# Kernel optimization log

Measured on AMD Instinct MI355X. Metric: run time of the kernel, lower is better.

Reference implementation:

```python
import jax, jax.numpy as jnp
import numpy as np

VOCAB = 32000
EMB = 512
HID = 1024
B = 64
LPRE = 256
MAXL = 16


def _gru(x, Wih, Whh, bih, bhh):
    # x: (B, T, E); torch GRU gate order r, z, n
    Bb, T, E = x.shape
    H = Whh.shape[1]
    xW = jnp.einsum('bte,ge->btg', x, Wih) + bih  # (B, T, 3H)
    def step(h, xt):
        gh = h @ Whh.T + bhh
        r = jax.nn.sigmoid(xt[:, :H] + gh[:, :H])
        z = jax.nn.sigmoid(xt[:, H:2 * H] + gh[:, H:2 * H])
        n = jnp.tanh(xt[:, 2 * H:] + r * gh[:, 2 * H:])
        h = (1.0 - z) * n + z * h
        return h, h
    h0 = jnp.zeros((Bb, H), x.dtype)
    hT, ys = jax.lax.scan(step, h0, jnp.swapaxes(xW, 0, 1))
    return jnp.swapaxes(ys, 0, 1), hT


def setup_inputs() -> dict:
    key = jax.random.key(0)
    ks = jax.random.split(key, 24)
    s = 0.02
    inp = {
        'pre_seq': jax.random.randint(ks[0], (B, LPRE), 0, VOCAB),
        'post_seq': jax.random.randint(ks[1], (B, LPRE), 0, VOCAB),
        'trg': jax.random.randint(ks[2], (B, MAXL), 0, 2),
        'emb': jax.random.normal(ks[3], (VOCAB, EMB), jnp.float32) * s,
        'Wih_pre': jax.random.normal(ks[4], (3 * HID, EMB), jnp.float32) * s,
        'Whh_pre': jax.random.normal(ks[5], (3 * HID, HID), jnp.float32) * s,
        'bih_pre': jnp.zeros((3 * HID,), jnp.float32),
        'bhh_pre': jnp.zeros((3 * HID,), jnp.float32),
        'Wih_post': jax.random.normal(ks[6], (3 * HID, EMB), jnp.float32) * s,
        'Whh_post': jax.random.normal(ks[7], (3 * HID, HID), jnp.float32) * s,
        'bih_post': jnp.zeros((3 * HID,), jnp.float32),
        'bhh_post': jnp.zeros((3 * HID,), jnp.float32),
        'fc_W': jax.random.normal(ks[8], (HID, 2 * HID), jnp.float32) * s,
        'fc_b': jnp.zeros((HID,), jnp.float32),
        'attn_W': jax.random.normal(ks[9], (HID, 2 * HID), jnp.float32) * s,
        'attn_b': jnp.zeros((HID,), jnp.float32),
        'v_W': jax.random.normal(ks[10], (1, HID), jnp.float32) * s,
        'fc1_W': jax.random.normal(ks[11], (HID, HID), jnp.float32) * s,
        'fc1_b': jnp.zeros((HID,), jnp.float32),
        'fc2_W': jax.random.normal(ks[12], (HID, 2 * HID), jnp.float32) * s,
        'fc2_b': jnp.zeros((HID,), jnp.float32),
        'fco_W': jax.random.normal(ks[13], (1, 2 * HID), jnp.float32) * s,
        'fco_b': jnp.zeros((1,), jnp.float32),
    }
    return inp


def reference(pre_seq, post_seq, trg, emb,
              Wih_pre, Whh_pre, bih_pre, bhh_pre,
              Wih_post, Whh_post, bih_post, bhh_post,
              fc_W, fc_b, attn_W, attn_b, v_W,
              fc1_W, fc1_b, fc2_W, fc2_b, fco_W, fco_b):
    bsz, len_pre = pre_seq.shape
    max_len = trg.shape[1]
    # Encoder (dropout = identity, eval mode)
    pre_e = emb[pre_seq]
    post_e = emb[post_seq]
    pre_out, pre_h = _gru(pre_e, Wih_pre, Whh_pre, bih_pre, bhh_pre)
    post_out, post_h = _gru(post_e, Wih_post, Whh_post, bih_post, bhh_post)
    enc_out = jnp.concatenate([pre_out, post_out], axis=1)  # (B, 2*Lp, H)
    hidden = jnp.tanh(jnp.concatenate([pre_h, post_h], axis=-1) @ fc_W.T + fc_b)  # (B, H)
    # Decoder: hidden is never updated in the original loop, so one step suffices;
    # the per-t result is identical and is broadcast over max_len.
    src_len = enc_out.shape[1]
    hid_rep = jnp.broadcast_to(hidden[:, None, :], (bsz, src_len, hidden.shape[-1]))
    energy = jnp.tanh(jnp.concatenate([hid_rep, enc_out], axis=-1) @ attn_W.T + attn_b)
    a = jax.nn.softmax(jnp.einsum('bsh,h->bs', energy, v_W[0]), axis=1)  # (B, S)
    weighted = jnp.einsum('bs,bsh->bh', a, enc_out)  # (B, H)
    o = jnp.tanh(hidden @ fc1_W.T + fc1_b)
    o = jnp.tanh(jnp.concatenate([o, weighted], axis=1) @ fc2_W.T + fc2_b)  # (B, H)
    o_rep = jnp.broadcast_to(o[:, None, :], (bsz, src_len, o.shape[-1]))
    feat = jax.nn.relu(jnp.concatenate([enc_out, o_rep], axis=-1))  # (B, S, 2H)
    logits = jnp.einsum('bsf,of->bso', feat, fco_W) + fco_b  # (B, S, 1)
    sig = jax.nn.sigmoid(logits)
    outputs_pre = jnp.broadcast_to(sig[:, None, :len_pre, :], (bsz, max_len, len_pre, 1))
    outputs_post = jnp.broadcast_to(sig[:, None, len_pre:, :], (bsz, max_len, len_pre, 1))
    return outputs_pre, outputs_post
```

## Files before the change

### kernel.cpp

```cpp
#include <hip/hip_runtime.h>
#include <math.h>

#define BATCH 64
#define LPRE 256
#define EMBD 512
#define HID 1024
#define G3 3072
#define SRC 512

typedef unsigned int uint32;
typedef unsigned long long u64;
typedef short bf16x8 __attribute__((ext_vector_type(8)));
typedef float f32x4 __attribute__((ext_vector_type(4)));
typedef uint32 u32x4 __attribute__((ext_vector_type(4)));

__device__ __forceinline__ float frcp_(float x) { return __builtin_amdgcn_rcpf(x); }
__device__ __forceinline__ float sigmoidf_(float x) {
    x = fminf(fmaxf(x, -30.f), 30.f);
    return frcp_(1.0f + __expf(-x));
}
__device__ __forceinline__ float tanhf_(float x) {
    x = fminf(fmaxf(x, -15.f), 15.f);
    float e = __expf(2.f * x);
    return (e - 1.f) * frcp_(e + 1.f);
}

__device__ __forceinline__ unsigned short f2bf(float f) {
    uint32 u = __float_as_uint(f);
    return (unsigned short)((u + 0x7fffu + ((u >> 16) & 1u)) >> 16);
}
__device__ __forceinline__ float bf2f(unsigned short s) { return __uint_as_float(((uint32)s) << 16); }
__device__ __forceinline__ void up2(uint32 u, float& f0, float& f1) {
    f0 = __uint_as_float(u << 16);
    f1 = __uint_as_float(u & 0xffff0000u);
}
__device__ __forceinline__ uint4 pack8(float4 a, float4 b) {
    uint4 w;
    w.x = (uint32)f2bf(a.x) | ((uint32)f2bf(a.y) << 16);
    w.y = (uint32)f2bf(a.z) | ((uint32)f2bf(a.w) << 16);
    w.z = (uint32)f2bf(b.x) | ((uint32)f2bf(b.y) << 16);
    w.w = (uint32)f2bf(b.z) | ((uint32)f2bf(b.w) << 16);
    return w;
}

__global__ __launch_bounds__(256) void kcvt(const float* __restrict__ src, int ld, int off,
                                            unsigned short* __restrict__ dst, int cols, int n) {
    int i = blockIdx.x * 256 + threadIdx.x;
    if (i >= n) return;
    int r = i / cols, c = i - r * cols;
    dst[i] = f2bf(src[(size_t)r * ld + off + c]);
}

__global__ __launch_bounds__(256) void kproj(const int* __restrict__ pre_seq,
                                             const int* __restrict__ post_seq, int t0,
                                             const float* __restrict__ emb,
                                             const unsigned short* __restrict__ Wihb,
                                             const float* __restrict__ bih_pre,
                                             const float* __restrict__ bih_post,
                                             unsigned short* __restrict__ xw, int chunk) {
    __shared__ uint4 Asl[4][128];
    __shared__ uint4 Bsl[4][128];
    __shared__ int tok[128];
    int gru = blockIdx.z;
    const int* seq = gru ? post_seq : pre_seq;
    const unsigned short* Wb = Wihb + (size_t)gru * G3 * EMBD;
    const float* bih = gru ? bih_post : bih_pre;
    unsigned short* xwout = xw + (size_t)gru * BATCH * chunk * G3;
    int tid = threadIdx.x;
    int row0 = blockIdx.x * 128, col0 = blockIdx.y * 128;
    if (tid < 128) {
        int rr = row0 + tid;
        tok[tid] = seq[(rr / chunk) * LPRE + t0 + (rr % chunk)];
    }
    __syncthreads();
    int lane = tid & 63, w = tid >> 6;
    int wm = w >> 1, wn = w & 1;
    int q = lane >> 4, m = lane & 15;
    int r0s = tid & 127, g0s = tid >> 7;
    int g1s = g0s + 2;
    f32x4 acc[4][4] = {};
    for (int kk = 0; kk < EMBD; kk += 32) {
        const float* a0p = emb + (size_t)tok[r0s] * EMBD + kk + g0s * 8;
        const float* a1p = emb + (size_t)tok[r0s] * EMBD + kk + g1s * 8;
        float4 av00 = *(const float4*)a0p, av01 = *(const float4*)(a0p + 4);
        float4 av10 = *(const float4*)a1p, av11 = *(const float4*)(a1p + 4);
        uint4 bv0 = *(const uint4*)(Wb + (size_t)(col0 + r0s) * EMBD + kk + g0s * 8);
        uint4 bv1 = *(const uint4*)(Wb + (size_t)(col0 + r0s) * EMBD + kk + g1s * 8);
        __syncthreads();
        Asl[g0s][r0s ^ (g0s << 2)] = pack8(av00, av01);
        Asl[g1s][r0s ^ (g1s << 2)] = pack8(av10, av11);
        Bsl[g0s][r0s ^ (g0s << 2)] = bv0;
        Bsl[g1s][r0s ^ (g1s << 2)] = bv1;
        __syncthreads();
        bf16x8 af[4], bfv[4];
#pragma unroll
        for (int i = 0; i < 4; i++) af[i] = *(bf16x8*)&Asl[q][(wm * 64 + i * 16 + m) ^ (q << 2)];
#pragma unroll
        for (int j = 0; j < 4; j++) bfv[j] = *(bf16x8*)&Bsl[q][(wn * 64 + j * 16 + m) ^ (q << 2)];
#pragma unroll
        for (int i = 0; i < 4; i++)
#pragma unroll
            for (int j = 0; j < 4; j++)
                acc[i][j] = __builtin_amdgcn_mfma_f32_16x16x32_bf16(af[i], bfv[j], acc[i][j], 0, 0, 0);
    }
#pragma unroll
    for (int i = 0; i < 4; i++)
#pragma unroll
        for (int j = 0; j < 4; j++)
#pragma unroll
            for (int reg = 0; reg < 4; reg++) {
                int row = row0 + wm * 64 + i * 16 + q * 4 + reg;
                int col = col0 + wn * 64 + j * 16 + m;
                xwout[(size_t)row * G3 + col] = f2bf(acc[i][j][reg] + bih[col]);
            }
}

__global__ __launch_bounds__(512, 2) void kstepP(unsigned short* __restrict__ hbp,
                                                 float* __restrict__ hf,
                                                 const unsigned short* __restrict__ Whhb,
                                                 const float* __restrict__ bhh0,
                                                 const float* __restrict__ bhh1,
                                                 const unsigned short* __restrict__ xw,
                                                 unsigned short* __restrict__ enc,
                                                 uint32* __restrict__ bar,
                                                 int t0, int chunk) {
    __shared__ float gl[8][32][3][17];
    __shared__ unsigned short hsh[32][16];
    int gru = blockIdx.z;
    int mh = blockIdx.y;
    int u0 = blockIdx.x * 16;
    int tid = threadIdx.x;
    int ks = tid >> 6;
    int lane = tid & 63;
    int q = lane >> 4, m = lane & 15;
    int bbase = mh * 32;
    const unsigned short* Wg = Whhb + (size_t)gru * G3 * HID;
    const float* bhh = gru ? bhh1 : bhh0;

    int dom = gru * 2 + mh;
    uint32* slots = bar + (size_t)dom * 128;
    uint32* gen = bar + 512 + (size_t)dom * 32;
    int sid = blockIdx.x;
    bool leader = (blockIdx.x == 0);

    bf16x8 bfrag[3][4];
#pragma unroll
    for (int g = 0; g < 3; ++g) {
        const unsigned short* pb = Wg + (size_t)(g * HID + u0 + m) * HID + ks * 128 + q * 8;
#pragma unroll
        for (int it = 0; it < 4; ++it) bfrag[g][it] = *(const bf16x8*)(pb + it * 32);
    }
#pragma unroll
    for (int g = 0; g < 3; ++g)
#pragma unroll
        for (int it = 0; it < 4; ++it) asm volatile("" : "+v"(bfrag[g][it]));

    int bl = tid >> 4, ul = tid & 15;
    int be = bbase + bl, ue = u0 + ul;
    float brr = bhh[ue], bzz = bhh[HID + ue], bnn = bhh[2 * HID + ue];
    unsigned short h16r = __hip_atomic_load(
        &hbp[(size_t)(((t0 & 1) * 2 + gru) * BATCH + be) * HID + ue],
        __ATOMIC_RELAXED, __HIP_MEMORY_SCOPE_AGENT);

    const unsigned short* xwb = xw + ((size_t)(gru * BATCH + be) * chunk) * G3;
    float xr = bf2f(xwb[ue]);
    float xz = bf2f(xwb[HID + ue]);
    float xn = bf2f(xwb[2 * HID + ue]);

    for (int tl = 0; tl < chunk; ++tl) {
        int t = t0 + tl;
        int p = t & 1;
        const unsigned short* hb = hbp + ((size_t)p * 2 + gru) * BATCH * HID;
        unsigned short* hob = hbp + ((size_t)(p ^ 1) * 2 + gru) * BATCH * HID;

        const unsigned short* pa0 = hb + (size_t)(bbase + m) * HID + ks * 128 + q * 8;
        const unsigned short* pa1 = pa0 + (size_t)16 * HID;
        u32x4 av0[4], av1[4];
#pragma unroll
        for (int it = 0; it < 4; ++it) {
            asm volatile("global_load_dwordx4 %0, %1, off sc0 sc1"
                         : "=v"(av0[it]) : "v"(pa0 + it * 32));
            asm volatile("global_load_dwordx4 %0, %1, off sc0 sc1"
                         : "=v"(av1[it]) : "v"(pa1 + it * 32));
        }
        asm volatile("s_waitcnt vmcnt(0)" ::: "memory");
        __builtin_amdgcn_sched_barrier(0);

        f32x4 acc[3][2] = {};
#pragma unroll
        for (int it = 0; it < 4; ++it)
#pragma unroll
            for (int g = 0; g < 3; ++g) {
                acc[g][0] = __builtin_amdgcn_mfma_f32_16x16x32_bf16(*(bf16x8*)&av0[it], bfrag[g][it], acc[g][0], 0, 0, 0);
                acc[g][1] = __builtin_amdgcn_mfma_f32_16x16x32_bf16(*(bf16x8*)&av1[it], bfrag[g][it], acc[g][1], 0, 0, 0);
            }
#pragma unroll
        for (int g = 0; g < 3; ++g)
#pragma unroll
            for (int reg = 0; reg < 4; ++reg) {
                gl[ks][q * 4 + reg][g][m] = acc[g][0][reg];
                gl[ks][16 + q * 4 + reg][g][m] = acc[g][1][reg];
            }
        __syncthreads();
        float ar = 0.f, az = 0.f, an = 0.f;
#pragma unroll
        for (int k2 = 0; k2 < 8; ++k2) {
            ar += gl[k2][bl][0][ul];
            az += gl[k2][bl][1][ul];
            an += gl[k2][bl][2][ul];
        }
        float r = sigmoidf_(xr + ar + brr);
        float z = sigmoidf_(xz + az + bzz);
        float n = tanhf_(xn + r * (an + bnn));
        float hnew = (1.f - z) * n + z * bf2f(h16r);
        unsigned short h16 = f2bf(hnew);
        h16r = h16;
        hsh[bl][ul] = h16;
        enc[((size_t)be * SRC + gru * LPRE + t) * HID + ue] = h16;
        if (t == LPRE - 1) hf[((size_t)gru * BATCH + be) * HID + ue] = hnew;
        __syncthreads();
        if (tid < 64) {
            int row = tid >> 1, half = tid & 1;
            u32x4 hv = *(const u32x4*)&hsh[row][half * 8];
            unsigned short* dst = hob + (size_t)(bbase + row) * HID + u0 + half * 8;
            asm volatile("global_store_dwordx4 %0, %1, off sc0 sc1"
                         :: "v"(dst), "v"(hv) : "memory");
        }
        if (tl < chunk - 1) {
            uint32 t1 = (uint32)(t + 1);
            if (tid < 64)
                asm volatile("s_waitcnt vmcnt(0)" ::: "memory");
            if (tid == 0)
                __hip_atomic_store(&slots[sid], t1, __ATOMIC_RELAXED, __HIP_MEMORY_SCOPE_AGENT);
            const unsigned short* xwn = xwb + (size_t)(tl + 1) * G3;
            xr = bf2f(xwn[ue]);
            xz = bf2f(xwn[HID + ue]);
            xn = bf2f(xwn[2 * HID + ue]);
            if (leader && tid < 64) {
                for (;;) {
                    uint32 s0 = __hip_atomic_load(&slots[tid], __ATOMIC_RELAXED, __HIP_MEMORY_SCOPE_AGENT);
                    if (__all(s0 >= t1)) break;
                    __builtin_amdgcn_s_sleep(1);
                }
                if (tid == 0)
                    __hip_atomic_store(gen, t1, __ATOMIC_RELAXED, __HIP_MEMORY_SCOPE_AGENT);
            }
            if (tid == 0) {
                while (__hip_atomic_load(gen, __ATOMIC_RELAXED, __HIP_MEMORY_SCOPE_AGENT) < t1)
                    __builtin_amdgcn_s_sleep(1);
            }
            __syncthreads();
        }
    }
}

__global__ __launch_bounds__(256) void kg64(const float* __restrict__ A1, int K1,
                                            const float* __restrict__ A2, int K2,
                                            const unsigned short* __restrict__ Wb,
                                            const float* __restrict__ bias,
                                            float* __restrict__ out, int N, int act) {
    __shared__ uint4 Asl[4][64];
    int tid = threadIdx.x;
    int col0 = blockIdx.x * 64;
    int lane = tid & 63, w = tid >> 6;
    int q = lane >> 4, m = lane & 15;
    int K = K1 + K2;
    int arow = tid >> 2, akg = tid & 3;
    const unsigned short* wp = Wb + (size_t)(col0 + w * 16 + m) * K + q * 8;
    f32x4 acc[4] = {};
    for (int kk = 0; kk < K; kk += 32) {
        int k0 = kk + akg * 8;
        const float* ap = (k0 < K1) ? (A1 + (size_t)arow * K1 + k0)
                                    : (A2 + (size_t)arow * K2 + (k0 - K1));
        float4 v0 = *(const float4*)ap;
        float4 v1 = *(const float4*)(ap + 4);
        __syncthreads();
        Asl[akg][arow ^ (akg << 2)] = pack8(v0, v1);
        __syncthreads();
        bf16x8 bfv = *(const bf16x8*)(wp + kk);
        bf16x8 af[4];
#pragma unroll
        for (int i = 0; i < 4; i++) af[i] = *(bf16x8*)&Asl[q][(i * 16 + m) ^ (q << 2)];
#pragma unroll
        for (int i = 0; i < 4; i++)
            acc[i] = __builtin_amdgcn_mfma_f32_16x16x32_bf16(af[i], bfv, acc[i], 0, 0, 0);
    }
    int j = col0 + w * 16 + m;
    float bv = bias ? bias[j] : 0.f;
#pragma unroll
    for (int i = 0; i < 4; i++)
#pragma unroll
        for (int reg = 0; reg < 4; reg++) {
            int b = i * 16 + q * 4 + reg;
            float v = acc[i][reg] + bv;
            if (act == 1) v = tanhf_(v);
            out[(size_t)b * N + j] = v;
        }
}

__global__ __launch_bounds__(256) void kattn(const unsigned short* __restrict__ enc,
                                             const unsigned short* __restrict__ Wb,
                                             const float* __restrict__ attn_b,
                                             const float* __restrict__ hidA,
                                             const float* __restrict__ vW,
                                             const float* __restrict__ fcoW,
                                             float* __restrict__ e,
                                             float* __restrict__ dvec) {
    __shared__ uint4 Asl[4][128];
    __shared__ uint4 Bsl[4][128];
    __shared__ float red[2][128][17];
    __shared__ float dred[128][2];
    __shared__ float fsh[HID];
    int tid = threadIdx.x;
    int row0 = blockIdx.x * 128, col0 = blockIdx.y * 128;
    bool dwork = (blockIdx.y == 0);
    if (dwork)
        for (int l = tid; l < HID; l += 256) fsh[l] = fcoW[l];
    int lane = tid & 63, w = tid >> 6;
    int wm = w >> 1, wn = w & 1;
    int q = lane >> 4, m = lane & 15;
    int r0s = tid & 127, g0s = tid >> 7;
    int g1s = g0s + 2;
    f32x4 acc[4][4] = {};
    float dacc = 0.f;
    for (int kk = 0; kk < HID; kk += 32) {
        uint4 av0 = *(const uint4*)(enc + (size_t)(row0 + r0s) * HID + kk + g0s * 8);
        uint4 av1 = *(const uint4*)(enc + (size_t)(row0 + r0s) * HID + kk + g1s * 8);
        uint4 bv0 = *(const uint4*)(Wb + (size_t)(col0 + r0s) * HID + kk + g0s * 8);
        uint4 bv1 = *(const uint4*)(Wb + (size_t)(col0 + r0s) * HID + kk + g1s * 8);
        __syncthreads();
        Asl[g0s][r0s ^ (g0s << 2)] = av0;
        Asl[g1s][r0s ^ (g1s << 2)] = av1;
        Bsl[g0s][r0s ^ (g0s << 2)] = bv0;
        Bsl[g1s][r0s ^ (g1s << 2)] = bv1;
        __syncthreads();
        bf16x8 af[4], bfv[4];
#pragma unroll
        for (int i = 0; i < 4; i++) af[i] = *(bf16x8*)&Asl[q][(wm * 64 + i * 16 + m) ^ (q << 2)];
#pragma unroll
        for (int j = 0; j < 4; j++) bfv[j] = *(bf16x8*)&Bsl[q][(wn * 64 + j * 16 + m) ^ (q << 2)];
        if (dwork) {
            int r2 = tid >> 1, sp = tid & 1;
#pragma unroll
            for (int sg = 0; sg < 2; sg++) {
                int seg = sp * 2 + sg;
                uint4 v = Asl[seg][r2 ^ (seg << 2)];
                const uint32* vw = (const uint32*)&v;
#pragma unroll
                for (int wd = 0; wd < 4; wd++) {
                    float e0, e1;
                    up2(vw[wd], e0, e1);
                    int kb = kk + seg * 8 + wd * 2;
                    dacc += fmaxf(e0, 0.f) * fsh[kb] + fmaxf(e1, 0.f) * fsh[kb + 1];
                }
            }
        }
#pragma unroll
        for (int i = 0; i < 4; i++)
#pragma unroll
            for (int j = 0; j < 4; j++)
                acc[i][j] = __builtin_amdgcn_mfma_f32_16x16x32_bf16(af[i], bfv[j], acc[i][j], 0, 0, 0);
    }
    int b = row0 / SRC;
#pragma unroll
    for (int i = 0; i < 4; i++)
#pragma unroll
        for (int reg = 0; reg < 4; reg++) {
            int row_local = wm * 64 + i * 16 + q * 4 + reg;
            float s = 0.f;
#pragma unroll
            for (int j = 0; j < 4; j++) {
                int col = col0 + wn * 64 + j * 16 + m;
                float v = acc[i][j][reg] + hidA[(size_t)b * HID + col] + attn_b[col];
                s += vW[col] * tanhf(v);
            }
            red[wn][row_local][m] = s;
        }
    if (dwork) dred[tid >> 1][tid & 1] = dacc;
    __syncthreads();
    if (tid < 128) {
        float s = 0.f;
        for (int c = 0; c < 16; c++) s += red[0][tid][c] + red[1][tid][c];
        atomicAdd(e + row0 + tid, s);
        if (dwork) dvec[row0 + tid] = dred[tid][0] + dred[tid][1];
    }
}

__global__ __launch_bounds__(256) void ksoftmax(const float* __restrict__ e, float* __restrict__ a) {
    int b = blockIdx.x;
    int tid = threadIdx.x;
    __shared__ float red[256];
    float v0 = e[(size_t)b * SRC + tid], v1 = e[(size_t)b * SRC + 256 + tid];
    red[tid] = fmaxf(v0, v1);
    __syncthreads();
    for (int st = 128; st > 0; st >>= 1) {
        if (tid < st) red[tid] = fmaxf(red[tid], red[tid + st]);
        __syncthreads();
    }
    float mx = red[0];
    __syncthreads();
    float e0 = __expf(v0 - mx), e1 = __expf(v1 - mx);
    red[tid] = e0 + e1;
    __syncthreads();
    for (int st = 128; st > 0; st >>= 1) {
        if (tid < st) red[tid] += red[tid + st];
        __syncthreads();
    }
    float inv = 1.0f / red[0];
    a[(size_t)b * SRC + tid] = e0 * inv;
    a[(size_t)b * SRC + 256 + tid] = e1 * inv;
}

__global__ __launch_bounds__(256) void kweighted(const float* __restrict__ a,
                                                 const unsigned short* __restrict__ enc,
                                                 float* __restrict__ wout) {
    int b = blockIdx.y;
    int h = blockIdx.x * 256 + threadIdx.x;
    __shared__ float as[512];
    for (int l = threadIdx.x; l < 512; l += 256) as[l] = a[(size_t)b * SRC + l];
    __syncthreads();
    float acc = 0.f;
    for (int s = 0; s < SRC; s++) acc += as[s] * bf2f(enc[((size_t)b * SRC + s) * HID + h]);
    wout[(size_t)b * HID + h] = acc;
}

__global__ __launch_bounds__(256) void koc(const float* __restrict__ o2,
                                           const float* __restrict__ fcoW,
                                           float* __restrict__ oc) {
    int b = blockIdx.x;
    int tid = threadIdx.x;
    __shared__ float red[256];
    float s = 0.f;
    for (int j = tid; j < HID; j += 256) s += fmaxf(o2[(size_t)b * HID + j], 0.f) * fcoW[HID + j];
    red[tid] = s;
    __syncthreads();
    for (int st = 128; st > 0; st >>= 1) {
        if (tid < st) red[tid] += red[tid + st];
        __syncthreads();
    }
    if (tid == 0) oc[b] = red[0];
}

__global__ __launch_bounds__(256) void kout(const float* __restrict__ dvec,
                                            const float* __restrict__ oc,
                                            const float* __restrict__ fcob,
                                            float* __restrict__ out) {
    int idx = blockIdx.x * 256 + threadIdx.x;
    int b = idx >> 9, s = idx & 511;
    float logit = dvec[idx] + oc[b] + fcob[0];
    float sig = frcp_(1.f + __expf(-fminf(fmaxf(logit, -30.f), 30.f)));
    size_t base = (s < LPRE) ? ((size_t)b * 4096 + s)
                             : (262144 + (size_t)b * 4096 + (s - 256));
    for (int l = 0; l < 16; l++) out[base + (size_t)l * 256] = sig;
}

extern "C" void kernel_launch(void* const* d_in, const int* in_sizes, int n_in,
                              void* d_out, int out_size, void* d_ws, size_t ws_size,
                              hipStream_t stream) {
    (void)in_sizes; (void)n_in; (void)out_size;
    const int* pre_seq = (const int*)d_in[0];
    const int* post_seq = (const int*)d_in[1];
    const float* emb = (const float*)d_in[3];
    const float* Wih_pre = (const float*)d_in[4];
    const float* Whh_pre = (const float*)d_in[5];
    const float* bih_pre = (const float*)d_in[6];
    const float* bhh_pre = (const float*)d_in[7];
    const float* Wih_post = (const float*)d_in[8];
    const float* Whh_post = (const float*)d_in[9];
    const float* bih_post = (const float*)d_in[10];
    const float* bhh_post = (const float*)d_in[11];
    const float* fc_W = (const float*)d_in[12];
    const float* fc_b = (const float*)d_in[13];
    const float* attn_W = (const float*)d_in[14];
    const float* attn_b = (const float*)d_in[15];
    const float* v_W = (const float*)d_in[16];
    const float* fc1_W = (const float*)d_in[17];
    const float* fc1_b = (const float*)d_in[18];
    const float* fc2_W = (const float*)d_in[19];
    const float* fc2_b = (const float*)d_in[20];
    const float* fco_W = (const float*)d_in[21];
    const float* fco_b = (const float*)d_in[22];
    float* out = (float*)d_out;

    const size_t fixed_bytes = 103420160ull + 65536;
    int CH = (ws_size >= fixed_bytes + (size_t)2 * BATCH * 64 * G3 * 2) ? 64 : 32;

    char* ws = (char*)d_ws;
    unsigned short* xw = (unsigned short*)ws;     ws += (size_t)2 * BATCH * CH * G3 * 2;
    unsigned short* enc = (unsigned short*)ws;    ws += (size_t)BATCH * SRC * HID * 2;
    unsigned short* hbp = (unsigned short*)ws;    ws += (size_t)2 * 2 * BATCH * HID * 2;
    float* hf = (float*)ws;                       ws += (size_t)2 * BATCH * HID * 4;
    unsigned short* Wihb = (unsigned short*)ws;   ws += (size_t)2 * G3 * EMBD * 2;
    unsigned short* Whhb = (unsigned short*)ws;   ws += (size_t)2 * G3 * HID * 2;
    unsigned short* attnWb = (unsigned short*)ws; ws += (size_t)HID * HID * 2;
    unsigned short* attnWa = (unsigned short*)ws; ws += (size_t)HID * HID * 2;
    unsigned short* fcWb = (unsigned short*)ws;   ws += (size_t)HID * 2 * HID * 2;
    unsigned short* fc1b = (unsigned short*)ws;   ws += (size_t)HID * HID * 2;
    unsigned short* fc2b = (unsigned short*)ws;   ws += (size_t)HID * 2 * HID * 2;
    uint32* bar = (uint32*)ws;                    ws += 4096;
    float* dvec = (float*)ws;                     ws += (size_t)BATCH * SRC * 4;
    float* hidden = (float*)ws;                   ws += (size_t)BATCH * HID * 4;
    float* hidA = (float*)ws;                     ws += (size_t)BATCH * HID * 4;
    float* evec = (float*)ws;                     ws += (size_t)BATCH * SRC * 4;
    float* avec = (float*)ws;                     ws += (size_t)BATCH * SRC * 4;
    float* wsum = (float*)ws;                     ws += (size_t)BATCH * HID * 4;
    float* o1 = (float*)ws;                       ws += (size_t)BATCH * HID * 4;
    float* o2 = (float*)ws;                       ws += (size_t)BATCH * HID * 4;
    float* oc = (float*)ws;                       ws += (size_t)BATCH * 4;

    hipMemsetAsync(hbp, 0, (size_t)2 * 2 * BATCH * HID * 2, stream);
    hipMemsetAsync(evec, 0, (size_t)BATCH * SRC * 4, stream);
    hipMemsetAsync(bar, 0, 4096, stream);

    {
        int n1 = G3 * EMBD;
        kcvt<<<(n1 + 255) / 256, 256, 0, stream>>>(Wih_pre, EMBD, 0, Wihb, EMBD, n1);
        kcvt<<<(n1 + 255) / 256, 256, 0, stream>>>(Wih_post, EMBD, 0, Wihb + (size_t)G3 * EMBD, EMBD, n1);
        int n2 = G3 * HID;
        kcvt<<<(n2 + 255) / 256, 256, 0, stream>>>(Whh_pre, HID, 0, Whhb, HID, n2);
        kcvt<<<(n2 + 255) / 256, 256, 0, stream>>>(Whh_post, HID, 0, Whhb + (size_t)G3 * HID, HID, n2);
        int n3 = HID * HID;
        kcvt<<<(n3 + 255) / 256, 256, 0, stream>>>(attn_W, 2 * HID, HID, attnWb, HID, n3);
        kcvt<<<(n3 + 255) / 256, 256, 0, stream>>>(attn_W, 2 * HID, 0, attnWa, HID, n3);
        kcvt<<<(n3 + 255) / 256, 256, 0, stream>>>(fc1_W, HID, 0, fc1b, HID, n3);
        int n4 = HID * 2 * HID;
        kcvt<<<(n4 + 255) / 256, 256, 0, stream>>>(fc_W, 2 * HID, 0, fcWb, 2 * HID, n4);
        kcvt<<<(n4 + 255) / 256, 256, 0, stream>>>(fc2_W, 2 * HID, 0, fc2b, 2 * HID, n4);
    }

    for (int c = 0; c < LPRE / CH; c++) {
        kproj<<<dim3(BATCH * CH / 128, G3 / 128, 2), 256, 0, stream>>>(
            pre_seq, post_seq, c * CH, emb, Wihb, bih_pre, bih_post, xw, CH);
        kstepP<<<dim3(64, 2, 2), 512, 0, stream>>>(hbp, hf, Whhb, bhh_pre, bhh_post,
                                                   xw, enc, bar, c * CH, CH);
    }
    float* pre_h = hf;
    float* post_h = hf + (size_t)BATCH * HID;

    kg64<<<HID / 64, 256, 0, stream>>>(pre_h, HID, post_h, HID, fcWb, fc_b, hidden, HID, 1);
    kg64<<<HID / 64, 256, 0, stream>>>(hidden, HID, (const float*)nullptr, 0, attnWa,
                                       (const float*)nullptr, hidA, HID, 0);
    kattn<<<dim3(BATCH * SRC / 128, HID / 128), 256, 0, stream>>>(enc, attnWb, attn_b, hidA,
                                                                  v_W, fco_W, evec, dvec);
    ksoftmax<<<BATCH, 256, 0, stream>>>(evec, avec);
    kweighted<<<dim3(HID / 256, BATCH), 256, 0, stream>>>(avec, enc, wsum);
    kg64<<<HID / 64, 256, 0, stream>>>(hidden, HID, (const float*)nullptr, 0, fc1b, fc1_b, o1, HID, 1);
    kg64<<<HID / 64, 256, 0, stream>>>(o1, HID, wsum, HID, fc2b, fc2_b, o2, HID, 1);
    koc<<<BATCH, 256, 0, stream>>>(o2, fco_W, oc);
    kout<<<BATCH * SRC / 256, 256, 0, stream>>>(dvec, oc, fco_b, out);
}
```

Measured before the change: 1.982 ms.

## Batch weight conversions into one kernel, pre-convert embedding, fuse softmax with weighted sum

Replaces nine separate fp32-to-bf16 conversion launches with one grid-stride kernel that walks a segment table and converts four floats per thread. When the workspace is large enough, it also converts the whole embedding table to bf16 up front, so kproj loads packed bf16 rows instead of converting gathered fp32 rows itself. Softmax and the attention-weighted sum are fused into one kernel that recomputes the softmax in every block. The cost is converting the full 32000x512 embedding table (much more than the 32768 rows actually gathered) plus redundant softmax work per block.

```diff
diff --git a/kernel.cpp b/kernel.cpp
--- a/kernel.cpp
+++ b/kernel.cpp
@@ -7,6 +7,7 @@
 #define HID 1024
 #define G3 3072
 #define SRC 512
+#define VOCAB 32000
 
 typedef unsigned int uint32;
 typedef unsigned long long u64;
@@ -30,10 +31,6 @@
     return (unsigned short)((u + 0x7fffu + ((u >> 16) & 1u)) >> 16);
 }
 __device__ __forceinline__ float bf2f(unsigned short s) { return __uint_as_float(((uint32)s) << 16); }
-__device__ __forceinline__ void up2(uint32 u, float& f0, float& f1) {
-    f0 = __uint_as_float(u << 16);
-    f1 = __uint_as_float(u & 0xffff0000u);
-}
 __device__ __forceinline__ uint4 pack8(float4 a, float4 b) {
     uint4 w;
     w.x = (uint32)f2bf(a.x) | ((uint32)f2bf(a.y) << 16);
@@ -42,18 +39,42 @@
     w.w = (uint32)f2bf(b.z) | ((uint32)f2bf(b.w) << 16);
     return w;
 }
-
-__global__ __launch_bounds__(256) void kcvt(const float* __restrict__ src, int ld, int off,
-                                            unsigned short* __restrict__ dst, int cols, int n) {
-    int i = blockIdx.x * 256 + threadIdx.x;
-    if (i >= n) return;
-    int r = i / cols, c = i - r * cols;
-    dst[i] = f2bf(src[(size_t)r * ld + off + c]);
+__device__ __forceinline__ void up2(uint32 u, float& f0, float& f1) {
+    f0 = __uint_as_float(u << 16);
+    f1 = __uint_as_float(u & 0xffff0000u);
+}
+
+struct CvtSeg { const float* src; unsigned short* dst; int ld, off, colshift; uint32 gend; };
+struct CvtArgs { CvtSeg s[10]; uint32 total; };
+
+__global__ __launch_bounds__(256) void kcvtN(CvtArgs a) {
+    uint32 stride = gridDim.x * 256;
+    for (uint32 g = blockIdx.x * 256 + threadIdx.x; g < a.total; g += stride) {
+        uint32 gs = 0;
+#pragma unroll
+        for (int k = 0; k < 10; k++) {
+            if (g < a.s[k].gend) {
+                uint32 lg = g - gs;
+                size_t e = (size_t)lg * 4;
+                int r = (int)(e >> a.s[k].colshift);
+                int c = (int)(e & (((size_t)1 << a.s[k].colshift) - 1));
+                const float* sp = a.s[k].src + (size_t)r * a.s[k].ld + a.s[k].off + c;
+                float4 v = *(const float4*)sp;
+                uint2 w;
+                w.x = (uint32)f2bf(v.x) | ((uint32)f2bf(v.y) << 16);
+                w.y = (uint32)f2bf(v.z) | ((uint32)f2bf(v.w) << 16);
+                *(uint2*)(a.s[k].dst + e) = w;
+                break;
+            }
+            gs = a.s[k].gend;
+        }
+    }
 }
 
 __global__ __launch_bounds__(256) void kproj(const int* __restrict__ pre_seq,
                                              const int* __restrict__ post_seq, int t0,
                                              const float* __restrict__ emb,
+                                             const unsigned short* __restrict__ embb,
                                              const unsigned short* __restrict__ Wihb,
                                              const float* __restrict__ bih_pre,
                                              const float* __restrict__ bih_post,
@@ -80,15 +101,23 @@
     int g1s = g0s + 2;
     f32x4 acc[4][4] = {};
     for (int kk = 0; kk < EMBD; kk += 32) {
-        const float* a0p = emb + (size_t)tok[r0s] * EMBD + kk + g0s * 8;
-        const float* a1p = emb + (size_t)tok[r0s] * EMBD + kk + g1s * 8;
-        float4 av00 = *(const float4*)a0p, av01 = *(const float4*)(a0p + 4);
-        float4 av10 = *(const float4*)a1p, av11 = *(const float4*)(a1p + 4);
+        uint4 apack0, apack1;
+        if (embb) {
+            apack0 = *(const uint4*)(embb + (size_t)tok[r0s] * EMBD + kk + g0s * 8);
+            apack1 = *(const uint4*)(embb + (size_t)tok[r0s] * EMBD + kk + g1s * 8);
+        } else {
+            const float* a0p = emb + (size_t)tok[r0s] * EMBD + kk + g0s * 8;
+            const float* a1p = emb + (size_t)tok[r0s] * EMBD + kk + g1s * 8;
+            float4 av00 = *(const float4*)a0p, av01 = *(const float4*)(a0p + 4);
+            float4 av10 = *(const float4*)a1p, av11 = *(const float4*)(a1p + 4);
+            apack0 = pack8(av00, av01);
+            apack1 = pack8(av10, av11);
+        }
         uint4 bv0 = *(const uint4*)(Wb + (size_t)(col0 + r0s) * EMBD + kk + g0s * 8);
         uint4 bv1 = *(const uint4*)(Wb + (size_t)(col0 + r0s) * EMBD + kk + g1s * 8);
         __syncthreads();
-        Asl[g0s][r0s ^ (g0s << 2)] = pack8(av00, av01);
-        Asl[g1s][r0s ^ (g1s << 2)] = pack8(av10, av11);
+        Asl[g0s][r0s ^ (g0s << 2)] = apack0;
+        Asl[g1s][r0s ^ (g1s << 2)] = apack1;
         Bsl[g0s][r0s ^ (g0s << 2)] = bv0;
         Bsl[g1s][r0s ^ (g1s << 2)] = bv1;
         __syncthreads();
@@ -386,11 +415,14 @@
     }
 }
 
-__global__ __launch_bounds__(256) void ksoftmax(const float* __restrict__ e, float* __restrict__ a) {
-    int b = blockIdx.x;
+__global__ __launch_bounds__(256) void kswW(const float* __restrict__ evec,
+                                            const unsigned short* __restrict__ enc,
+                                            float* __restrict__ wout) {
+    __shared__ float red[256];
+    __shared__ float asw[512];
+    int b = blockIdx.y;
     int tid = threadIdx.x;
-    __shared__ float red[256];
-    float v0 = e[(size_t)b * SRC + tid], v1 = e[(size_t)b * SRC + 256 + tid];
+    float v0 = evec[(size_t)b * SRC + tid], v1 = evec[(size_t)b * SRC + 256 + tid];
     red[tid] = fmaxf(v0, v1);
     __syncthreads();
     for (int st = 128; st > 0; st >>= 1) {
@@ -407,20 +439,12 @@
         __syncthreads();
     }
     float inv = 1.0f / red[0];
-    a[(size_t)b * SRC + tid] = e0 * inv;
-    a[(size_t)b * SRC + 256 + tid] = e1 * inv;
-}
-
-__global__ __launch_bounds__(256) void kweighted(const float* __restrict__ a,
-                                                 const unsigned short* __restrict__ enc,
-                                                 float* __restrict__ wout) {
-    int b = blockIdx.y;
-    int h = blockIdx.x * 256 + threadIdx.x;
-    __shared__ float as[512];
-    for (int l = threadIdx.x; l < 512; l += 256) as[l] = a[(size_t)b * SRC + l];
-    __syncthreads();
+    asw[tid] = e0 * inv;
+    asw[tid + 256] = e1 * inv;
+    __syncthreads();
+    int h = blockIdx.x * 256 + tid;
     float acc = 0.f;
-    for (int s = 0; s < SRC; s++) acc += as[s] * bf2f(enc[((size_t)b * SRC + s) * HID + h]);
+    for (int s = 0; s < SRC; s++) acc += asw[s] * bf2f(enc[((size_t)b * SRC + s) * HID + h]);
     wout[(size_t)b * HID + h] = acc;
 }
 
@@ -507,30 +531,46 @@
     float* o1 = (float*)ws;                       ws += (size_t)BATCH * HID * 4;
     float* o2 = (float*)ws;                       ws += (size_t)BATCH * HID * 4;
     float* oc = (float*)ws;                       ws += (size_t)BATCH * 4;
+    (void)avec;
+    size_t emb_bytes = (size_t)VOCAB * EMBD * 2;
+    unsigned short* embb = (unsigned short*)ws;
+    int use_embb = ((size_t)((char*)(ws + 0) + emb_bytes - (char*)d_ws) <= ws_size) ? 1 : 0;
 
     hipMemsetAsync(hbp, 0, (size_t)2 * 2 * BATCH * HID * 2, stream);
     hipMemsetAsync(evec, 0, (size_t)BATCH * SRC * 4, stream);
     hipMemsetAsync(bar, 0, 4096, stream);
 
     {
-        int n1 = G3 * EMBD;
-        kcvt<<<(n1 + 255) / 256, 256, 0, stream>>>(Wih_pre, EMBD, 0, Wihb, EMBD, n1);
-        kcvt<<<(n1 + 255) / 256, 256, 0, stream>>>(Wih_post, EMBD, 0, Wihb + (size_t)G3 * EMBD, EMBD, n1);
-        int n2 = G3 * HID;
-        kcvt<<<(n2 + 255) / 256, 256, 0, stream>>>(Whh_pre, HID, 0, Whhb, HID, n2);
-        kcvt<<<(n2 + 255) / 256, 256, 0, stream>>>(Whh_post, HID, 0, Whhb + (size_t)G3 * HID, HID, n2);
-        int n3 = HID * HID;
-        kcvt<<<(n3 + 255) / 256, 256, 0, stream>>>(attn_W, 2 * HID, HID, attnWb, HID, n3);
-        kcvt<<<(n3 + 255) / 256, 256, 0, stream>>>(attn_W, 2 * HID, 0, attnWa, HID, n3);
-        kcvt<<<(n3 + 255) / 256, 256, 0, stream>>>(fc1_W, HID, 0, fc1b, HID, n3);
-        int n4 = HID * 2 * HID;
-        kcvt<<<(n4 + 255) / 256, 256, 0, stream>>>(fc_W, 2 * HID, 0, fcWb, 2 * HID, n4);
-        kcvt<<<(n4 + 255) / 256, 256, 0, stream>>>(fc2_W, 2 * HID, 0, fc2b, 2 * HID, n4);
-    }
-
+        CvtArgs a;
+        uint32 cum = 0;
+        int k = 0;
+        auto add = [&](const float* src, unsigned short* dst, int ld, int off, int colshift, uint32 ngrp) {
+            cum += ngrp;
+            a.s[k].src = src; a.s[k].dst = dst; a.s[k].ld = ld; a.s[k].off = off;
+            a.s[k].colshift = colshift; a.s[k].gend = cum; k++;
+        };
+        if (use_embb) add(emb, embb, EMBD, 0, 9, (uint32)(VOCAB * EMBD / 4));
+        add(Wih_pre, Wihb, EMBD, 0, 9, G3 * EMBD / 4);
+        add(Wih_post, Wihb + (size_t)G3 * EMBD, EMBD, 0, 9, G3 * EMBD / 4);
+        add(Whh_pre, Whhb, HID, 0, 10, G3 * HID / 4);
+        add(Whh_post, Whhb + (size_t)G3 * HID, HID, 0, 10, G3 * HID / 4);
+        add(attn_W, attnWb, 2 * HID, HID, 10, HID * HID / 4);
+        add(attn_W, attnWa, 2 * HID, 0, 10, HID * HID / 4);
+        add(fc1_W, fc1b, HID, 0, 10, HID * HID / 4);
+        add(fc_W, fcWb, 2 * HID, 0, 11, HID * 2 * HID / 4);
+        add(fc2_W, fc2b, 2 * HID, 0, 11, HID * 2 * HID / 4);
+        while (k < 10) {
+            a.s[k].src = Wih_pre; a.s[k].dst = Wihb; a.s[k].ld = EMBD; a.s[k].off = 0;
+            a.s[k].colshift = 9; a.s[k].gend = cum; k++;
+        }
+        a.total = cum;
+        kcvtN<<<2048, 256, 0, stream>>>(a);
+    }
+
+    const unsigned short* embb_arg = use_embb ? embb : (const unsigned short*)nullptr;
     for (int c = 0; c < LPRE / CH; c++) {
         kproj<<<dim3(BATCH * CH / 128, G3 / 128, 2), 256, 0, stream>>>(
-            pre_seq, post_seq, c * CH, emb, Wihb, bih_pre, bih_post, xw, CH);
+            pre_seq, post_seq, c * CH, emb, embb_arg, Wihb, bih_pre, bih_post, xw, CH);
         kstepP<<<dim3(64, 2, 2), 512, 0, stream>>>(hbp, hf, Whhb, bhh_pre, bhh_post,
                                                    xw, enc, bar, c * CH, CH);
     }
@@ -542,8 +582,7 @@
                                        (const float*)nullptr, hidA, HID, 0);
     kattn<<<dim3(BATCH * SRC / 128, HID / 128), 256, 0, stream>>>(enc, attnWb, attn_b, hidA,
                                                                   v_W, fco_W, evec, dvec);
-    ksoftmax<<<BATCH, 256, 0, stream>>>(evec, avec);
-    kweighted<<<dim3(HID / 256, BATCH), 256, 0, stream>>>(avec, enc, wsum);
+    kswW<<<dim3(HID / 256, BATCH), 256, 0, stream>>>(evec, enc, wsum);
     kg64<<<HID / 64, 256, 0, stream>>>(hidden, HID, (const float*)nullptr, 0, fc1b, fc1_b, o1, HID, 1);
     kg64<<<HID / 64, 256, 0, stream>>>(o1, HID, wsum, HID, fc2b, fc2_b, o2, HID, 1);
     koc<<<BATCH, 256, 0, stream>>>(o2, fco_W, oc);
```

New measurement: 1.872 ms, median of 2. -5.6%, faster.
